# Performance work log

Hardware: AMD Instinct MI355X
Metric: run time of the kernel (lower is better)

The kernel has to match this reference:

```python
import jax, jax.numpy as jnp
import numpy as np
import math

E = 1024   # embed_size
H = 16     # heads arg (actual per-'head' dim due to source's reshape quirk)
G = E // H # 64 head-groups (treated as heads in the source code)
FF = 4 * E


def setup_inputs() -> dict:
    key = jax.random.key(0)
    ks = jax.random.split(key, 12)
    s = 1.0 / math.sqrt(E)
    inp = {
        'x': jax.random.normal(ks[0], (2, 1024, E), dtype=jnp.float32),
        # linear weights stored as (in, out); torch Linear computes x @ W.T + b
        'Wq': jax.random.uniform(ks[1], (E, E), jnp.float32, -s, s),
        'Wk': jax.random.uniform(ks[2], (E, E), jnp.float32, -s, s),
        'Wv': jax.random.uniform(ks[3], (E, E), jnp.float32, -s, s),
        'Wo': jax.random.uniform(ks[4], (E, E), jnp.float32, -s, s),
        'bo': jax.random.uniform(ks[5], (E,), jnp.float32, -s, s),
        'W1': jax.random.uniform(ks[6], (E, FF), jnp.float32, -s, s),
        'b1': jax.random.uniform(ks[7], (FF,), jnp.float32, -s, s),
        'W2': jax.random.uniform(ks[8], (FF, E), jnp.float32, -1.0 / math.sqrt(FF), 1.0 / math.sqrt(FF)),
        'b2': jax.random.uniform(ks[9], (E,), jnp.float32, -s, s),
        'g1': jnp.ones((E,), jnp.float32), 'be1': jnp.zeros((E,), jnp.float32),
        'g2': jnp.ones((E,), jnp.float32), 'be2': jnp.zeros((E,), jnp.float32),
    }
    return inp


def _layernorm(x, g, b, eps=1e-5):
    mu = jnp.mean(x, axis=-1, keepdims=True)
    var = jnp.mean(jnp.square(x - mu), axis=-1, keepdims=True)
    return (x - mu) * jax.lax.rsqrt(var + eps) * g + b


def reference(x, Wq, Wk, Wv, Wo, bo, W1, b1, W2, b2, g1, be1, g2, be2):
    B, S, _ = x.shape
    # QKV projections; faithful to source: split E into (G=E//H groups, H dims),
    # group axis acts as the 'head' axis, per-head dim is H, scale = sqrt(H).
    def split(t):  # [B,S,E] -> [B,G,S,H]
        return t.reshape(B, S, G, H).transpose(0, 2, 1, 3)
    q = split(x @ Wq)
    k = split(x @ Wk)
    v = split(x @ Wv)
    att = jnp.einsum('bgsh,bgth->bgst', q, k) / math.sqrt(H)
    causal = jnp.tril(jnp.ones((S, S), dtype=bool))  # mask==1 above diag -> -inf
    att = jnp.where(causal, att, -jnp.inf)
    att = jax.nn.softmax(att, axis=-1)
    y = jnp.einsum('bgst,bgth->bgsh', att, v)          # [B,G,S,H]
    y = y.transpose(0, 2, 1, 3).reshape(B, S, E)
    attn_out = y @ Wo + bo
    # dropout is identity at inference
    x = _layernorm(attn_out + x, g1, be1)
    ff = jax.nn.relu(x @ W1 + b1) @ W2 + b2
    x = _layernorm(ff + x, g2, be2)
    return x
```

## Files before the change

### kernel.cpp

```cpp
#include <hip/hip_runtime.h>
#include <hip/hip_bf16.h>
#include <math.h>


#define E_DIM 1024
#define S_LEN 1024
#define B_SZ  2
#define G_HEADS 64
#define H_DIM 16
#define FF_DIM 4096
#define M_ROWS (B_SZ * S_LEN)
#define QKV_N  (3 * E_DIM)

#define QSCALE 0.36067376022224085f

#if __has_builtin(__builtin_amdgcn_exp2f)
  #define EXP2(x) __builtin_amdgcn_exp2f(x)
#else
  #define EXP2(x) __expf((x) * 0.6931471805599453f)
#endif

#define VT_STRIDE 136
#define VT_BUF    2312

using bf16x8 = __attribute__((ext_vector_type(8))) short;
using f32x4  = __attribute__((ext_vector_type(4))) float;
using f32x16 = __attribute__((ext_vector_type(16))) float;
using ushort8 = __attribute__((ext_vector_type(8))) unsigned short;

static __device__ __forceinline__ unsigned short f2bf(float f) {
    union { float f; unsigned int u; } x; x.f = f;
    unsigned int r = x.u + 0x7fff + ((x.u >> 16) & 1);
    return (unsigned short)(r >> 16);
}
static __device__ __forceinline__ unsigned int pack2(float a, float b) {
    union { __hip_bfloat162 h; unsigned int u; } c;
    c.h = __float22bfloat162_rn(float2{a, b});
    return c.u;
}

__global__ __launch_bounds__(256) void prep_kernel(
    const float* __restrict__ x,
    const float* __restrict__ Wq, const float* __restrict__ Wk,
    const float* __restrict__ Wv, const float* __restrict__ Wo,
    const float* __restrict__ W1_, const float* __restrict__ W2_,
    unsigned short* __restrict__ xb, unsigned short* __restrict__ Wqkt,
    unsigned short* __restrict__ Wot, unsigned short* __restrict__ W1t,
    unsigned short* __restrict__ W2t)
{
    const int id = blockIdx.x;
    if (id < 1024) {
        const size_t i = ((size_t)id * 256 + threadIdx.x) * 8;
        float4 a = *(const float4*)(x + i);
        float4 b = *(const float4*)(x + i + 4);
        ushort8 o;
        o[0] = f2bf(a.x); o[1] = f2bf(a.y); o[2] = f2bf(a.z); o[3] = f2bf(a.w);
        o[4] = f2bf(b.x); o[5] = f2bf(b.y); o[6] = f2bf(b.z); o[7] = f2bf(b.w);
        *(ushort8*)(xb + i) = o;
        return;
    }

    __shared__ float tile[32][33];
    const float* W; unsigned short* Wt; int N, K, n0, k0;
    if (id < 5120) {
        const int q = id - 1024;
        const int z = q >> 10;
        W  = (z == 0) ? Wq : (z == 1) ? Wk : (z == 2) ? Wv : Wo;
        Wt = (z < 3) ? (Wqkt + (size_t)z * E_DIM * E_DIM) : Wot;
        N = E_DIM; K = E_DIM;
        n0 = (q & 31) * 32; k0 = ((q >> 5) & 31) * 32;
    } else {
        const int q = id - 5120;
        const int z = q >> 12;
        const int qx = q & 4095;
        const int bx = qx & 127, by = qx >> 7;
        W  = z ? W2_ : W1_;
        Wt = z ? W2t : W1t;
        N  = z ? E_DIM : FF_DIM;
        K  = z ? FF_DIM : E_DIM;
        n0 = (z ? by : bx) * 32;
        k0 = (z ? bx : by) * 32;
    }
    const int t = threadIdx.x;
    const int r = t >> 3;
    const int c = (t & 7) * 4;

    float4 v = *(const float4*)(W + (size_t)(k0 + r) * N + n0 + c);
    tile[r][c] = v.x; tile[r][c + 1] = v.y; tile[r][c + 2] = v.z; tile[r][c + 3] = v.w;
    __syncthreads();

    ushort4 o;
    o.x = f2bf(tile[c + 0][r]); o.y = f2bf(tile[c + 1][r]);
    o.z = f2bf(tile[c + 2][r]); o.w = f2bf(tile[c + 3][r]);
    *(ushort4*)(Wt + (size_t)(n0 + r) * K + k0 + c) = o;
}

template<int ACT, int OUTBF, int SCALEQ, int NT>
__global__ __launch_bounds__(256) void gemm_mfma(
    const unsigned short* __restrict__ A,
    const unsigned short* __restrict__ Bt,
    const float* __restrict__ bias,
    float* __restrict__ C0, float* __restrict__ C1,
    unsigned short* __restrict__ Cb,
    int Krow, int Kchunk, int ldc)
{
    constexpr int NFR   = NT / 32;
    constexpr int BSUB  = NT * 32;
    constexpr int SUBSZ = 4096 + BSUB;
    __shared__ __align__(16) unsigned short lds[2][2 * SUBSZ];

    const int tid  = threadIdx.x;
    const int wave = tid >> 6;
    const int lane = tid & 63;
    const int wr = wave >> 1;
    const int wc = wave & 1;
    const int row0 = blockIdx.y * 128;
    const int col0 = blockIdx.x * NT;
    const int kbase = blockIdx.z * Kchunk;

    const int lr = lane & 15;
    const int lk = (lane >> 4) * 8;

    const int srow = (lane >> 2);
    const int scol = (lane & 3) * 8;

    f32x4 acc[4][NFR] = {};

    auto STAGE1 = [&](unsigned short* dstA, unsigned short* dstB, int k0) {
        #pragma unroll
        for (int i = 0; i < 2; ++i) {
            const int ci = wave + i * 4;
            const unsigned short* src =
                A + (size_t)(row0 + ci * 16 + srow) * Krow + k0 + scol;
            __builtin_amdgcn_global_load_lds(
                (const __attribute__((address_space(1))) void*)src,
                (__attribute__((address_space(3))) void*)(dstA + ci * 512),
                16, 0, 0);
        }
        #pragma unroll
        for (int i = 0; i < NFR / 2; ++i) {
            const int ci = wave + i * 4;
            const unsigned short* src =
                Bt + (size_t)(col0 + ci * 16 + srow) * Krow + k0 + scol;
            __builtin_amdgcn_global_load_lds(
                (const __attribute__((address_space(1))) void*)src,
                (__attribute__((address_space(3))) void*)(dstB + ci * 512),
                16, 0, 0);
        }
    };
    auto STAGE = [&](int buf, int k0) {
        STAGE1(&lds[buf][0],     &lds[buf][4096],         k0);
        STAGE1(&lds[buf][SUBSZ], &lds[buf][SUBSZ + 4096], k0 + 32);
    };
    auto COMPUTE = [&](int buf, int sub) {
        const unsigned short* As = &lds[buf][sub * SUBSZ];
        const unsigned short* Bs = As + 4096;
        bf16x8 a[4], b[NFR];
        #pragma unroll
        for (int mi = 0; mi < 4; ++mi)
            a[mi] = *(const bf16x8*)(As + (wr * 64 + mi * 16 + lr) * 32 + lk);
        #pragma unroll
        for (int ni = 0; ni < NFR; ++ni)
            b[ni] = *(const bf16x8*)(Bs + (wc * (NT / 2) + ni * 16 + lr) * 32 + lk);
        #pragma unroll
        for (int mi = 0; mi < 4; ++mi)
            #pragma unroll
            for (int ni = 0; ni < NFR; ++ni)
                acc[mi][ni] = __builtin_amdgcn_mfma_f32_16x16x32_bf16(
                    a[mi], b[ni], acc[mi][ni], 0, 0, 0);
    };

    const int nt = Kchunk >> 6;

    STAGE(0, kbase);
    asm volatile("s_waitcnt vmcnt(0)" ::: "memory");
    __builtin_amdgcn_s_barrier();

    int cur = 0;
    for (int t = 0; t < nt; ++t) {
        if (t + 1 < nt) STAGE(cur ^ 1, kbase + (t + 1) * 64);
        COMPUTE(cur, 0);
        COMPUTE(cur, 1);
        asm volatile("s_waitcnt vmcnt(0)" ::: "memory");
        __builtin_amdgcn_s_barrier();
        cur ^= 1;
    }

    float* Cw = blockIdx.z ? C1 : C0;
    #pragma unroll
    for (int mi = 0; mi < 4; ++mi) {
        #pragma unroll
        for (int ni = 0; ni < NFR; ++ni) {
            const int cc  = col0 + wc * (NT / 2) + ni * 16 + (lane & 15);
            const int rr0 = row0 + wr * 64 + mi * 16 + ((lane >> 4) << 2);
            const float bv = bias ? bias[cc] : 0.f;
            #pragma unroll
            for (int j = 0; j < 4; ++j) {
                float v = acc[mi][ni][j] + bv;
                if (ACT == 1) v = fmaxf(v, 0.f);
                if (SCALEQ && cc < E_DIM) v *= QSCALE;
                if (OUTBF) Cb[(size_t)(rr0 + j) * ldc + cc] = f2bf(v);
                else       Cw[(size_t)(rr0 + j) * ldc + cc] = v;
            }
        }
    }
}

__global__ __launch_bounds__(256) void attn_kernel(
    const unsigned short* __restrict__ qkv, unsigned short* __restrict__ Yb)
{
    __shared__ __align__(16) unsigned short Ks[2][2048];
    __shared__ __align__(16) unsigned short Vt[2][VT_BUF];

    const int bi = blockIdx.x >> 7;
    const int bg = blockIdx.x & 127;
    const int g  = bg & (G_HEADS - 1);
    const int b  = bg >> 6;
    const int tid  = threadIdx.x;
    const int lane = tid & 63;
    const int l31  = lane & 31;
    const int hi   = lane >> 5;
    const int wv   = tid >> 6;
    const int tokb = b * S_LEN;

    const int cblk = 28 - 4 * bi;
    const int q0   = (cblk + wv) * 32;
    const int qrow = q0 + l31;
    const int nt128 = (cblk + 4) >> 2;

    const bf16x8 qf = *(const bf16x8*)(
        qkv + (size_t)(tokb + qrow) * QKV_N + g * H_DIM + hi * 8);

    f32x16 acc = {};
    const f32x16 fz = {};

    const int kv  = tid >> 7;
    const int lw  = (tid >> 6) & 1;
    const int skey0 = lw * 32 + (lane >> 1);
    const int shalf = lane & 1;
    const size_t sgo = (size_t)(g * H_DIM + (1 + kv) * E_DIM + shalf * 8);

    auto STAGE = [&](int buf, int t128, ushort8* vreg) {
        #pragma unroll
        for (int i = 0; i < 2; ++i) {
            const unsigned short* src =
                qkv + (size_t)(tokb + t128 * 128 + skey0 + i * 64) * QKV_N + sgo;
            if (kv == 0) {
                __builtin_amdgcn_global_load_lds(
                    (const __attribute__((address_space(1))) void*)src,
                    (__attribute__((address_space(3))) void*)(
                        &Ks[buf][(lw * 64 + i * 128) * 8]),
                    16, 0, 0);
            } else {
                vreg[i] = *(const ushort8*)src;
            }
        }
    };
    auto WRITE_V = [&](int buf, const ushort8* vreg) {
        if (kv == 1) {
            #pragma unroll
            for (int i = 0; i < 2; ++i)
                #pragma unroll
                for (int j = 0; j < 8; ++j)
                    Vt[buf][(shalf * 8 + j) * VT_STRIDE + skey0 + i * 64] =
                        vreg[i][j];
        }
    };

    const int vrow = (l31 == 16) ? 16 : (l31 & 15);

    auto PROCESS = [&](int cur, int sub, int t0) {
        const bf16x8 kf = *(const bf16x8*)(&Ks[cur][(sub * 32 + l31) * 16 + hi * 8]);
        __builtin_amdgcn_s_setprio(1);
        f32x16 s = __builtin_amdgcn_mfma_f32_32x32x16_bf16(kf, qf, fz, 0, 0, 0);
        __builtin_amdgcn_s_setprio(0);

        float pq[16];
        if (t0 == q0) {
            #pragma unroll
            for (int r = 0; r < 16; ++r) {
                const int key = t0 + (r & 3) + 8 * (r >> 2) + 4 * hi;
                pq[r] = (key > qrow) ? 0.f : EXP2(s[r]);
            }
        } else {
            #pragma unroll
            for (int r = 0; r < 16; ++r) pq[r] = EXP2(s[r]);
        }

        unsigned int cw[8];
        #pragma unroll
        for (int r2 = 0; r2 < 8; ++r2) cw[r2] = pack2(pq[2 * r2], pq[2 * r2 + 1]);

        union { uint4 u; bf16x8 v; } pf0, pf1;
        {
            unsigned int a = cw[0], c = cw[2];
            asm volatile("v_permlane32_swap_b32 %0, %1" : "+v"(a), "+v"(c));
            pf0.u.x = a; pf0.u.z = c;
        }
        {
            unsigned int a = cw[1], c = cw[3];
            asm volatile("v_permlane32_swap_b32 %0, %1" : "+v"(a), "+v"(c));
            pf0.u.y = a; pf0.u.w = c;
        }
        {
            unsigned int a = cw[4], c = cw[6];
            asm volatile("v_permlane32_swap_b32 %0, %1" : "+v"(a), "+v"(c));
            pf1.u.x = a; pf1.u.z = c;
        }
        {
            unsigned int a = cw[5], c = cw[7];
            asm volatile("v_permlane32_swap_b32 %0, %1" : "+v"(a), "+v"(c));
            pf1.u.y = a; pf1.u.w = c;
        }

        const unsigned short* vbase =
            &Vt[cur][vrow * VT_STRIDE + sub * 32 + hi * 8];
        const bf16x8 vb0 = *(const bf16x8*)(vbase);
        const bf16x8 vb1 = *(const bf16x8*)(vbase + 16);

        __builtin_amdgcn_s_setprio(1);
        acc = __builtin_amdgcn_mfma_f32_32x32x16_bf16(pf0.v, vb0, acc, 0, 0, 0);
        acc = __builtin_amdgcn_mfma_f32_32x32x16_bf16(pf1.v, vb1, acc, 0, 0, 0);
        __builtin_amdgcn_s_setprio(0);
    };

    ushort8 vreg[2] = {};
    STAGE(0, 0, vreg);
    if (kv == 1) {
        const int vt = tid - 128;
        Vt[0][16 * VT_STRIDE + vt] = 0x3F80;
        Vt[1][16 * VT_STRIDE + vt] = 0x3F80;
    }
    WRITE_V(0, vreg);
    __syncthreads();

    int cur = 0;
    for (int t = 0; t < nt128; ++t) {
        ushort8 vnext[2] = {};
        const bool more = (t + 1 < nt128);
        if (more) STAGE(cur ^ 1, t + 1, vnext);
        #pragma unroll
        for (int sub = 0; sub < 4; ++sub) {
            const int t0 = t * 128 + sub * 32;
            if (t0 <= q0) PROCESS(cur, sub, t0);
        }
        if (more) WRITE_V(cur ^ 1, vnext);
        asm volatile("s_waitcnt vmcnt(0) lgkmcnt(0)" ::: "memory");
        __builtin_amdgcn_s_barrier();
        cur ^= 1;
    }

    float linv[16];
    #pragma unroll
    for (int r = 0; r < 16; ++r) {
        const float lr_ = __shfl(acc[r], (hi << 5) + 16);
        linv[r] = __builtin_amdgcn_rcpf(lr_);
    }
    if (l31 < H_DIM) {
        #pragma unroll
        for (int r = 0; r < 16; ++r) {
            const int q = (r & 3) + 8 * (r >> 2) + 4 * hi;
            Yb[(size_t)(tokb + q0 + q) * E_DIM + g * H_DIM + l31] =
                f2bf(acc[r] * linv[r]);
        }
    }
}

__global__ __launch_bounds__(256) void add_ln2_kernel(
    const float* __restrict__ P0, const float* __restrict__ P1,
    const float* __restrict__ bias, const float* __restrict__ resid,
    const float* __restrict__ g, const float* __restrict__ be,
    float* __restrict__ O, unsigned short* __restrict__ Ob)
{
    const int row = blockIdx.x;
    const size_t base = (size_t)row * E_DIM;
    const int tid = threadIdx.x;

    float v[4];
    float s = 0.f;
    #pragma unroll
    for (int i = 0; i < 4; ++i) {
        int c = tid + i * 256;
        v[i] = P0[base + c] + P1[base + c] + bias[c] + resid[base + c];
        s += v[i];
    }

    __shared__ float red[256];
    red[tid] = s; __syncthreads();
    for (int st = 128; st >= 1; st >>= 1) {
        if (tid < st) red[tid] += red[tid + st];
        __syncthreads();
    }
    const float mu = red[0] * (1.f / E_DIM);
    __syncthreads();

    float s2 = 0.f;
    #pragma unroll
    for (int i = 0; i < 4; ++i) { float d = v[i] - mu; s2 += d * d; }
    red[tid] = s2; __syncthreads();
    for (int st = 128; st >= 1; st >>= 1) {
        if (tid < st) red[tid] += red[tid + st];
        __syncthreads();
    }
    const float rs = rsqrtf(red[0] * (1.f / E_DIM) + 1e-5f);

    #pragma unroll
    for (int i = 0; i < 4; ++i) {
        int c = tid + i * 256;
        float o = (v[i] - mu) * rs * g[c] + be[c];
        O[base + c] = o;
        if (Ob) Ob[base + c] = f2bf(o);
    }
}

extern "C" void kernel_launch(void* const* d_in, const int* in_sizes, int n_in,
                              void* d_out, int out_size, void* d_ws, size_t ws_size,
                              hipStream_t stream)
{
    const float* x  = (const float*)d_in[0];
    const float* Wq = (const float*)d_in[1];
    const float* Wk = (const float*)d_in[2];
    const float* Wv = (const float*)d_in[3];
    const float* Wo = (const float*)d_in[4];
    const float* bo = (const float*)d_in[5];
    const float* W1 = (const float*)d_in[6];
    const float* b1 = (const float*)d_in[7];
    const float* W2 = (const float*)d_in[8];
    const float* b2 = (const float*)d_in[9];
    const float* g1  = (const float*)d_in[10];
    const float* be1 = (const float*)d_in[11];
    const float* g2  = (const float*)d_in[12];
    const float* be2 = (const float*)d_in[13];

    char* W = (char*)d_ws;
    const size_t MB = 1024 * 1024;
    unsigned short* xb   = (unsigned short*)(W + 0 * MB);
    unsigned short* Wqkt = (unsigned short*)(W + 4 * MB);
    unsigned short* qkvb = (unsigned short*)(W + 10 * MB);
    unsigned short* yb   = (unsigned short*)(W + 22 * MB);
    unsigned short* Wot  = (unsigned short*)(W + 26 * MB);
    float* P_o0          = (float*)(W + 4 * MB);
    float* P_o1          = (float*)(W + 12 * MB);
    unsigned short* x1b  = (unsigned short*)(W + 20 * MB);
    float* x1            = (float*)(W + 28 * MB);
    unsigned short* W1t  = (unsigned short*)(W + 36 * MB);
    unsigned short* W2t  = (unsigned short*)(W + 44 * MB);
    unsigned short* ff1b = (unsigned short*)(W + 0 * MB);
    float* P_f1          = (float*)(W + 16 * MB);
    float* out           = (float*)d_out;

    dim3 blk(256);

    prep_kernel<<<dim3(13312), blk, 0, stream>>>(
        x, Wq, Wk, Wv, Wo, W1, W2, xb, Wqkt, Wot, W1t, W2t);
    gemm_mfma<0, 1, 1, 128><<<dim3(QKV_N / 128, M_ROWS / 128, 1), blk, 0, stream>>>(
        xb, Wqkt, nullptr, nullptr, nullptr, qkvb, E_DIM, E_DIM, QKV_N);
    attn_kernel<<<dim3(B_SZ * G_HEADS * 8), blk, 0, stream>>>(qkvb, yb);
    gemm_mfma<0, 0, 0, 64><<<dim3(E_DIM / 64, M_ROWS / 128, 2), blk, 0, stream>>>(
        yb, Wot, nullptr, P_o0, P_o1, nullptr, E_DIM, E_DIM / 2, E_DIM);
    add_ln2_kernel<<<dim3(M_ROWS), blk, 0, stream>>>(P_o0, P_o1, bo, x, g1, be1, x1, x1b);
    gemm_mfma<1, 1, 0, 128><<<dim3(FF_DIM / 128, M_ROWS / 128, 1), blk, 0, stream>>>(
        x1b, W1t, b1, nullptr, nullptr, ff1b, E_DIM, E_DIM, FF_DIM);
    gemm_mfma<0, 0, 0, 64><<<dim3(E_DIM / 64, M_ROWS / 128, 2), blk, 0, stream>>>(
        ff1b, W2t, nullptr, out, P_f1, nullptr, FF_DIM, FF_DIM / 2, E_DIM);
    add_ln2_kernel<<<dim3(M_ROWS), blk, 0, stream>>>(out, P_f1, b2, x1, g2, be2, out, nullptr);
}
```

Measured before the change: 144.2 us.

## Use 4-way split-K with 128-wide tiles for FFN down-projection and bf16 residual

The second FFN GEMM now uses 128-column tiles with a 4-way split-K instead of 64-column tiles with 2-way split. A new add_ln4 kernel sums the four partials. The residual for the second layernorm is read from the bf16 copy of x1, so the fp32 x1 write and later read are removed. This raises partial-sum traffic and loses precision in the residual in exchange for better per-block reuse and less fp32 traffic.

```diff
diff --git a/kernel.cpp b/kernel.cpp
--- a/kernel.cpp
+++ b/kernel.cpp
@@ -32,6 +32,10 @@
     union { float f; unsigned int u; } x; x.f = f;
     unsigned int r = x.u + 0x7fff + ((x.u >> 16) & 1);
     return (unsigned short)(r >> 16);
+}
+static __device__ __forceinline__ float bf2f(unsigned short u) {
+    union { unsigned int u; float f; } x; x.u = ((unsigned int)u) << 16;
+    return x.f;
 }
 static __device__ __forceinline__ unsigned int pack2(float a, float b) {
     union { __hip_bfloat162 h; unsigned int u; } c;
@@ -101,6 +105,7 @@
     const unsigned short* __restrict__ Bt,
     const float* __restrict__ bias,
     float* __restrict__ C0, float* __restrict__ C1,
+    float* __restrict__ C2, float* __restrict__ C3,
     unsigned short* __restrict__ Cb,
     int Krow, int Kchunk, int ldc)
 {
@@ -186,7 +191,8 @@
         cur ^= 1;
     }
 
-    float* Cw = blockIdx.z ? C1 : C0;
+    const int z = blockIdx.z;
+    float* Cw = (z == 0) ? C0 : (z == 1) ? C1 : (z == 2) ? C2 : C3;
     #pragma unroll
     for (int mi = 0; mi < 4; ++mi) {
         #pragma unroll
@@ -408,8 +414,55 @@
     for (int i = 0; i < 4; ++i) {
         int c = tid + i * 256;
         float o = (v[i] - mu) * rs * g[c] + be[c];
-        O[base + c] = o;
+        if (O)  O[base + c] = o;
         if (Ob) Ob[base + c] = f2bf(o);
+    }
+}
+
+__global__ __launch_bounds__(256) void add_ln4_kernel(
+    const float* __restrict__ P0, const float* __restrict__ P1,
+    const float* __restrict__ P2, const float* __restrict__ P3,
+    const float* __restrict__ bias, const unsigned short* __restrict__ residb,
+    const float* __restrict__ g, const float* __restrict__ be,
+    float* __restrict__ O)
+{
+    const int row = blockIdx.x;
+    const size_t base = (size_t)row * E_DIM;
+    const int tid = threadIdx.x;
+
+    float v[4];
+    float s = 0.f;
+    #pragma unroll
+    for (int i = 0; i < 4; ++i) {
+        int c = tid + i * 256;
+        v[i] = P0[base + c] + P1[base + c] + P2[base + c] + P3[base + c]
+             + bias[c] + bf2f(residb[base + c]);
+        s += v[i];
+    }
+
+    __shared__ float red[256];
+    red[tid] = s; __syncthreads();
+    for (int st = 128; st >= 1; st >>= 1) {
+        if (tid < st) red[tid] += red[tid + st];
+        __syncthreads();
+    }
+    const float mu = red[0] * (1.f / E_DIM);
+    __syncthreads();
+
+    float s2 = 0.f;
+    #pragma unroll
+    for (int i = 0; i < 4; ++i) { float d = v[i] - mu; s2 += d * d; }
+    red[tid] = s2; __syncthreads();
+    for (int st = 128; st >= 1; st >>= 1) {
+        if (tid < st) red[tid] += red[tid + st];
+        __syncthreads();
+    }
+    const float rs = rsqrtf(red[0] * (1.f / E_DIM) + 1e-5f);
+
+    #pragma unroll
+    for (int i = 0; i < 4; ++i) {
+        int c = tid + i * 256;
+        O[base + c] = (v[i] - mu) * rs * g[c] + be[c];
     }
 }
 
@@ -442,11 +495,12 @@
     float* P_o0          = (float*)(W + 4 * MB);
     float* P_o1          = (float*)(W + 12 * MB);
     unsigned short* x1b  = (unsigned short*)(W + 20 * MB);
-    float* x1            = (float*)(W + 28 * MB);
     unsigned short* W1t  = (unsigned short*)(W + 36 * MB);
     unsigned short* W2t  = (unsigned short*)(W + 44 * MB);
     unsigned short* ff1b = (unsigned short*)(W + 0 * MB);
-    float* P_f1          = (float*)(W + 16 * MB);
+    float* P_f1          = (float*)(W + 52 * MB);
+    float* P_f2          = (float*)(W + 60 * MB);
+    float* P_f3          = (float*)(W + 68 * MB);
     float* out           = (float*)d_out;
 
     dim3 blk(256);
@@ -454,14 +508,20 @@
     prep_kernel<<<dim3(13312), blk, 0, stream>>>(
         x, Wq, Wk, Wv, Wo, W1, W2, xb, Wqkt, Wot, W1t, W2t);
     gemm_mfma<0, 1, 1, 128><<<dim3(QKV_N / 128, M_ROWS / 128, 1), blk, 0, stream>>>(
-        xb, Wqkt, nullptr, nullptr, nullptr, qkvb, E_DIM, E_DIM, QKV_N);
+        xb, Wqkt, nullptr, nullptr, nullptr, nullptr, nullptr, qkvb,
+        E_DIM, E_DIM, QKV_N);
     attn_kernel<<<dim3(B_SZ * G_HEADS * 8), blk, 0, stream>>>(qkvb, yb);
     gemm_mfma<0, 0, 0, 64><<<dim3(E_DIM / 64, M_ROWS / 128, 2), blk, 0, stream>>>(
-        yb, Wot, nullptr, P_o0, P_o1, nullptr, E_DIM, E_DIM / 2, E_DIM);
-    add_ln2_kernel<<<dim3(M_ROWS), blk, 0, stream>>>(P_o0, P_o1, bo, x, g1, be1, x1, x1b);
+        yb, Wot, nullptr, P_o0, P_o1, nullptr, nullptr, nullptr,
+        E_DIM, E_DIM / 2, E_DIM);
+    add_ln2_kernel<<<dim3(M_ROWS), blk, 0, stream>>>(
+        P_o0, P_o1, bo, x, g1, be1, nullptr, x1b);
     gemm_mfma<1, 1, 0, 128><<<dim3(FF_DIM / 128, M_ROWS / 128, 1), blk, 0, stream>>>(
-        x1b, W1t, b1, nullptr, nullptr, ff1b, E_DIM, E_DIM, FF_DIM);
-    gemm_mfma<0, 0, 0, 64><<<dim3(E_DIM / 64, M_ROWS / 128, 2), blk, 0, stream>>>(
-        ff1b, W2t, nullptr, out, P_f1, nullptr, FF_DIM, FF_DIM / 2, E_DIM);
-    add_ln2_kernel<<<dim3(M_ROWS), blk, 0, stream>>>(out, P_f1, b2, x1, g2, be2, out, nullptr);
-}
+        x1b, W1t, b1, nullptr, nullptr, nullptr, nullptr, ff1b,
+        E_DIM, E_DIM, FF_DIM);
+    gemm_mfma<0, 0, 0, 128><<<dim3(E_DIM / 128, M_ROWS / 128, 4), blk, 0, stream>>>(
+        ff1b, W2t, nullptr, out, P_f1, P_f2, P_f3, nullptr,
+        FF_DIM, FF_DIM / 4, E_DIM);
+    add_ln4_kernel<<<dim3(M_ROWS), blk, 0, stream>>>(
+        out, P_f1, P_f2, P_f3, b2, x1b, g2, be2, out);
+}
```

Result: no change. 143.4 us (median of 2 runs) (-0.6%).
